# Performance work log

Measured on AMD Instinct MI355X. Metric: run time of the kernel, lower is better.

The kernel has to match this reference:

```python
import jax, jax.numpy as jnp
import numpy as np

N_NODES = 50000
N_EDGES = 800000
IN_FEAT = 100
OUT_FEAT = 100
NUM_RELS = 200
NUM_HEADS = 3
NUM_BASES = 100
SUB_IN = 1   # in_feat // num_bases
SUB_OUT = 1  # out_feat // num_bases


def setup_inputs() -> dict:
    key = jax.random.key(0)
    ks = jax.random.split(key, 10)
    return {
        "h": jax.random.normal(ks[0], (N_NODES, IN_FEAT), jnp.float32),
        "e": jax.random.normal(ks[1], (N_EDGES, IN_FEAT), jnp.float32),
        "norm": jax.random.uniform(ks[2], (N_NODES, 1), jnp.float32),
        "weight": jax.random.normal(ks[3], (NUM_RELS, NUM_BASES * SUB_IN * SUB_OUT), jnp.float32) * 0.1,
        "attn": jax.random.normal(ks[4], (NUM_RELS, NUM_HEADS, OUT_FEAT), jnp.float32) * 0.1,
        "fc_w": jax.random.normal(ks[5], (IN_FEAT, OUT_FEAT * NUM_HEADS), jnp.float32) * 0.1,
        "loop_w": jax.random.normal(ks[6], (IN_FEAT, OUT_FEAT), jnp.float32) * 0.1,
        "rel": jax.random.randint(ks[7], (N_EDGES,), 0, NUM_RELS, jnp.int32),
        "src": jax.random.randint(ks[8], (N_EDGES,), 0, N_NODES, jnp.int32),
        "dst": jax.random.randint(ks[9], (N_EDGES,), 0, N_NODES, jnp.int32),
    }


def reference(h, e, norm, weight, attn, fc_w, loop_w, rel, src, dst):
    E = rel.shape[0]
    # --- relation-indexed block-diagonal message (torch.bmm over blocks) ---
    W_e = weight[rel].reshape(E, NUM_BASES, SUB_IN, SUB_OUT)        # per-edge block weights
    h_src = h[src].reshape(E, NUM_BASES, SUB_IN)                    # gathered src features
    msg = jnp.einsum('ebi,ebio->ebo', h_src, W_e).reshape(E, OUT_FEAT)
    # --- edge-feature attention fuse ---
    a_e = attn[rel]                                                 # (E, H, OUT)
    fc_e = (e @ fc_w).reshape(E, NUM_HEADS, OUT_FEAT)               # fc(edge)
    feat = jax.nn.leaky_relu(a_e * fc_e, 0.2).sum(axis=1)           # (E, OUT)
    msg = msg + feat
    # --- scatter-sum aggregation to dst nodes, then norm + self-loop ---
    agg = jax.ops.segment_sum(msg, dst, num_segments=N_NODES)       # (N, OUT)
    node = agg * norm
    loop_message = h @ loop_w
    return node + loop_message
```

## Files before the change

### kernel.cpp

```cpp
#include <hip/hip_runtime.h>
#include <hip/hip_bf16.h>

#define N_NODES 50000
#define N_EDGES 800000
#define IN_FEAT 100
#define OUT_FEAT 100
#define NUM_RELS 200
#define NUM_HEADS 3

#define KP 128
#define NPH 112
#define MB  128
#define NT_O 7
#define WPB 8
#define MSGW 100
#define BROWS 312
#define HSTRIDE 25600

#define WS_B       0u
#define WS_LW      86016u
#define WS_CNT     114688u
#define WS_OFFS    315392u
#define WS_CURSOR  516096u
#define WS_BSUM    716800u
#define WS_SLOT    717056u
#define WS_META    3917056u
#define WS_MSG     7117056u
#define WS_NEEDED  167117056u
#define NNODES_PAD 50176

typedef __attribute__((ext_vector_type(8))) short short8;
typedef __attribute__((ext_vector_type(4))) float f32x4;

__device__ __forceinline__ unsigned short f2bf(float f) {
    unsigned u = __builtin_bit_cast(unsigned, f);
    unsigned r = u + 0x7FFFu + ((u >> 16) & 1u);
    return (unsigned short)(r >> 16);
}
__device__ __forceinline__ float bf2f(unsigned hs) {
    return __builtin_bit_cast(float, hs << 16);
}

__global__ __launch_bounds__(256) void build_B(const float* __restrict__ fc_w,
                                               unsigned short* __restrict__ Bws) {
    int idx = blockIdx.x * 256 + threadIdx.x;
    if (idx >= BROWS * 16) return;
    int n = idx >> 4, g = idx & 15;
    int head = n / 100, nl = n - head * 100;
    int kt = g >> 2, g4 = g & 3;
    unsigned p[4] = {0u, 0u, 0u, 0u};
    if (n < 300) {
#pragma unroll
        for (int half = 0; half < 2; ++half) {
#pragma unroll
            for (int jp = 0; jp < 2; ++jp) {
                int k_lo = kt * 32 + half * 16 + g4 * 4 + jp * 2;
                int k_hi = k_lo + 1;
                float vlo = (k_lo < IN_FEAT)
                          ? fc_w[k_lo * (OUT_FEAT * NUM_HEADS) + head * OUT_FEAT + nl] : 0.f;
                float vhi = (k_hi < IN_FEAT)
                          ? fc_w[k_hi * (OUT_FEAT * NUM_HEADS) + head * OUT_FEAT + nl] : 0.f;
                p[half * 2 + jp] = (unsigned)f2bf(vlo) | ((unsigned)f2bf(vhi) << 16);
            }
        }
    }
    unsigned off = (unsigned)(n * 256) + (((unsigned)(g * 16)) ^ (((unsigned)(nl & 7)) << 4));
    *reinterpret_cast<int4*>(reinterpret_cast<char*>(Bws) + off) =
        make_int4((int)p[0], (int)p[1], (int)p[2], (int)p[3]);
}

__global__ __launch_bounds__(256) void build_LW(const float* __restrict__ loop_w,
                                                unsigned short* __restrict__ LWws) {
    int idx = blockIdx.x * 256 + threadIdx.x;
    if (idx >= NPH * 16) return;
    int nl = idx >> 4, g = idx & 15;
    int kt = g >> 2, g4 = g & 3;
    unsigned p[4];
#pragma unroll
    for (int half = 0; half < 2; ++half) {
#pragma unroll
        for (int jp = 0; jp < 2; ++jp) {
            int k_lo = kt * 32 + half * 16 + g4 * 4 + jp * 2;
            int k_hi = k_lo + 1;
            float vlo = (k_lo < IN_FEAT && nl < OUT_FEAT) ? loop_w[k_lo * OUT_FEAT + nl] : 0.f;
            float vhi = (k_hi < IN_FEAT && nl < OUT_FEAT) ? loop_w[k_hi * OUT_FEAT + nl] : 0.f;
            p[half * 2 + jp] = (unsigned)f2bf(vlo) | ((unsigned)f2bf(vhi) << 16);
        }
    }
    reinterpret_cast<int4*>(LWws)[idx] = make_int4((int)p[0], (int)p[1], (int)p[2], (int)p[3]);
}

__global__ __launch_bounds__(512, 2) void loop_gemm(const float* __restrict__ h,
                                                    const unsigned short* __restrict__ LWimg,
                                                    float* __restrict__ out) {
    const int tid = threadIdx.x;
    const int wave = tid >> 6, lane = tid & 63;
    const int lrow = lane & 15, lk = lane >> 4;
    const int rbase = blockIdx.x * MB;
    const int grow = rbase + wave * 16 + lrow;
    const bool ok = grow < N_NODES;
    const float* ap = h + (size_t)grow * IN_FEAT;

    short8 afrag[4];
#pragma unroll
    for (int kt = 0; kt < 4; ++kt) {
        int k0 = kt * 32 + lk * 4, k1 = k0 + 16;
        float4 va = (ok && k0 + 4 <= IN_FEAT) ? *reinterpret_cast<const float4*>(ap + k0)
                                              : make_float4(0.f, 0.f, 0.f, 0.f);
        float4 vb = (ok && k1 + 4 <= IN_FEAT) ? *reinterpret_cast<const float4*>(ap + k1)
                                              : make_float4(0.f, 0.f, 0.f, 0.f);
        afrag[kt][0] = (short)f2bf(va.x); afrag[kt][1] = (short)f2bf(va.y);
        afrag[kt][2] = (short)f2bf(va.z); afrag[kt][3] = (short)f2bf(va.w);
        afrag[kt][4] = (short)f2bf(vb.x); afrag[kt][5] = (short)f2bf(vb.y);
        afrag[kt][6] = (short)f2bf(vb.z); afrag[kt][7] = (short)f2bf(vb.w);
    }

#pragma unroll
    for (int nt = 0; nt < NT_O; ++nt) {
        f32x4 acc = (f32x4){0.f, 0.f, 0.f, 0.f};
#pragma unroll
        for (int kt = 0; kt < 4; ++kt) {
            short8 bfrag = *reinterpret_cast<const short8*>(
                LWimg + ((nt * 16 + lrow) * KP + kt * 32 + lk * 8));
            acc = __builtin_amdgcn_mfma_f32_16x16x32_bf16(afrag[kt], bfrag, acc, 0, 0, 0);
        }
        int o = nt * 16 + lrow;
        if (o < OUT_FEAT) {
#pragma unroll
            for (int r = 0; r < 4; ++r) {
                int crow = rbase + wave * 16 + lk * 4 + r;
                if (crow < N_NODES) out[(size_t)crow * OUT_FEAT + o] = acc[r];
            }
        }
    }
}

__global__ __launch_bounds__(512) void hist_kernel(const int* __restrict__ dst,
                                                   int* __restrict__ cnt) {
    int e = blockIdx.x * 512 + threadIdx.x;
    if (e < N_EDGES) atomicAdd(&cnt[dst[e]], 1);
}

__global__ __launch_bounds__(1024) void scan1(const int* __restrict__ cnt,
                                              int* __restrict__ offs,
                                              int* __restrict__ bsum) {
    __shared__ int s[1024];
    int i = blockIdx.x * 1024 + threadIdx.x;
    int v = (i < N_NODES) ? cnt[i] : 0;
    s[threadIdx.x] = v;
    __syncthreads();
    for (int d = 1; d < 1024; d <<= 1) {
        int t = (threadIdx.x >= d) ? s[threadIdx.x - d] : 0;
        __syncthreads();
        s[threadIdx.x] += t;
        __syncthreads();
    }
    offs[i] = s[threadIdx.x] - v;
    if (threadIdx.x == 1023) bsum[blockIdx.x] = s[1023];
}

__global__ __launch_bounds__(64) void scan2(int* __restrict__ bsum) {
    __shared__ int s[64];
    int v = (threadIdx.x < NNODES_PAD / 1024) ? bsum[threadIdx.x] : 0;
    s[threadIdx.x] = v;
    __syncthreads();
    for (int d = 1; d < 64; d <<= 1) {
        int t = (threadIdx.x >= d) ? s[threadIdx.x - d] : 0;
        __syncthreads();
        s[threadIdx.x] += t;
        __syncthreads();
    }
    bsum[threadIdx.x] = s[threadIdx.x] - v;
}

__global__ __launch_bounds__(1024) void scan3(int* __restrict__ offs,
                                              const int* __restrict__ bsum,
                                              int* __restrict__ cursor) {
    int i = blockIdx.x * 1024 + threadIdx.x;
    int v = offs[i] + bsum[blockIdx.x];
    offs[i] = v;
    cursor[i] = v;
}

__global__ __launch_bounds__(512) void scatter_kernel(const int* __restrict__ dst,
                                                      const int* __restrict__ src,
                                                      const int* __restrict__ rel,
                                                      int* __restrict__ cursor,
                                                      int* __restrict__ slotmap,
                                                      int* __restrict__ meta) {
    int e = blockIdx.x * 512 + threadIdx.x;
    if (e < N_EDGES) {
        int p = atomicAdd(&cursor[dst[e]], 1);
        slotmap[e] = p;
        meta[p] = (src[e] & 0xFFFF) | (rel[e] << 16);
    }
}

template<bool TOWS>
__global__ __launch_bounds__(512, 2) void feat_kernel(
        const float* __restrict__ efeat, const int* __restrict__ rel,
        const unsigned short* __restrict__ Bimg, const float* __restrict__ attn,
        const float* __restrict__ h, const float* __restrict__ weight,
        const float* __restrict__ norm, const int* __restrict__ src,
        const int* __restrict__ dst, const int* __restrict__ slotmap,
        float* __restrict__ out, unsigned short* __restrict__ msgws,
        int ntiles) {

    __shared__ __align__(16) unsigned short Blds[BROWS * 128];

    const int tid = threadIdx.x;
    {
        const int4* sp = reinterpret_cast<const int4*>(Bimg);
        int4* dp = reinterpret_cast<int4*>(Blds);
        for (int i = tid; i < BROWS * 128 / 8; i += 512) dp[i] = sp[i];
    }
    __syncthreads();

    const int wave = tid >> 6, lane = tid & 63;
    const int lrow = lane & 15, lk = lane >> 4;
    const int gstride = gridDim.x * WPB;
    int tile = blockIdx.x * WPB + wave;
    if (tile >= ntiles) return;

    const char* Bc = reinterpret_cast<const char*>(Blds);
    int bkt[4];
#pragma unroll
    for (int kt = 0; kt < 4; ++kt)
        bkt[kt] = lrow * 256 + ((kt * 64 + lk * 16) ^ ((lrow & 7) << 4));

    float4 pa[8];
    int prl[4];
    {
        const float* ap = efeat + (size_t)(tile * 16 + lrow) * IN_FEAT;
#pragma unroll
        for (int kt = 0; kt < 4; ++kt) {
            int k0 = kt * 32 + lk * 4, k1 = k0 + 16;
            pa[kt * 2]     = (k0 + 4 <= IN_FEAT) ? *reinterpret_cast<const float4*>(ap + k0)
                                                 : make_float4(0.f, 0.f, 0.f, 0.f);
            pa[kt * 2 + 1] = (k1 + 4 <= IN_FEAT) ? *reinterpret_cast<const float4*>(ap + k1)
                                                 : make_float4(0.f, 0.f, 0.f, 0.f);
        }
        const int* rp = rel + tile * 16 + lk * 4;
#pragma unroll
        for (int r = 0; r < 4; ++r) prl[r] = rp[r];
    }

    while (true) {
        const int cur = tile;
        const int tb = cur * 16;
        short8 afrag[4];
#pragma unroll
        for (int kt = 0; kt < 4; ++kt) {
            float4 va = pa[kt * 2], vb = pa[kt * 2 + 1];
            afrag[kt][0] = (short)f2bf(va.x); afrag[kt][1] = (short)f2bf(va.y);
            afrag[kt][2] = (short)f2bf(va.z); afrag[kt][3] = (short)f2bf(va.w);
            afrag[kt][4] = (short)f2bf(vb.x); afrag[kt][5] = (short)f2bf(vb.y);
            afrag[kt][6] = (short)f2bf(vb.z); afrag[kt][7] = (short)f2bf(vb.w);
        }
        int aoff[4];
#pragma unroll
        for (int r = 0; r < 4; ++r) aoff[r] = prl[r] * (NUM_HEADS * OUT_FEAT);

        int slot_r[4];
        if (TOWS) {
#pragma unroll
            for (int r = 0; r < 4; ++r) slot_r[r] = slotmap[tb + lk * 4 + r];
        }

        int next = tile + gstride;
        bool more = next < ntiles;
        {
            int pidx = more ? next : cur;
            const float* ap = efeat + (size_t)(pidx * 16 + lrow) * IN_FEAT;
#pragma unroll
            for (int kt = 0; kt < 4; ++kt) {
                int k0 = kt * 32 + lk * 4, k1 = k0 + 16;
                pa[kt * 2]     = (k0 + 4 <= IN_FEAT) ? *reinterpret_cast<const float4*>(ap + k0)
                                                     : make_float4(0.f, 0.f, 0.f, 0.f);
                pa[kt * 2 + 1] = (k1 + 4 <= IN_FEAT) ? *reinterpret_cast<const float4*>(ap + k1)
                                                     : make_float4(0.f, 0.f, 0.f, 0.f);
            }
            const int* rp = rel + pidx * 16 + lk * 4;
#pragma unroll
            for (int r = 0; r < 4; ++r) prl[r] = rp[r];
        }

        float feat[NT_O][4];
#pragma unroll
        for (int nt = 0; nt < NT_O; ++nt)
#pragma unroll
            for (int r = 0; r < 4; ++r) feat[nt][r] = 0.f;

#pragma unroll 1
        for (int hh = 0; hh < NUM_HEADS; ++hh) {
            const char* Bh = Bc + hh * HSTRIDE;
#pragma unroll
            for (int nt = 0; nt < NT_O; ++nt) {
                f32x4 acc = (f32x4){0.f, 0.f, 0.f, 0.f};
#pragma unroll
                for (int kt = 0; kt < 4; ++kt) {
                    short8 bfrag = *reinterpret_cast<const short8*>(
                        Bh + bkt[kt] + nt * 4096);
                    acc = __builtin_amdgcn_mfma_f32_16x16x32_bf16(afrag[kt], bfrag, acc, 0, 0, 0);
                }
                int o = nt * 16 + lrow;
                if (o < OUT_FEAT) {
                    int oo = hh * OUT_FEAT + o;
#pragma unroll
                    for (int r = 0; r < 4; ++r) {
                        float v = acc[r] * attn[aoff[r] + oo];
                        feat[nt][r] += (v > 0.f) ? v : 0.2f * v;
                    }
                }
            }
        }

        if (TOWS) {
#pragma unroll
            for (int nt = 0; nt < NT_O; ++nt) {
                int o = nt * 16 + lrow;
                if (o < OUT_FEAT) {
#pragma unroll
                    for (int r = 0; r < 4; ++r)
                        msgws[(size_t)slot_r[r] * MSGW + o] = f2bf(feat[nt][r]);
                }
            }
        } else {
            int sr_r[4], d_r[4]; float nm_r[4]; int rl_r[4];
#pragma unroll
            for (int r = 0; r < 4; ++r) {
                int ei = tb + lk * 4 + r;
                sr_r[r] = src[ei]; d_r[r] = dst[ei]; nm_r[r] = norm[d_r[r]];
                rl_r[r] = aoff[r] / (NUM_HEADS * OUT_FEAT);
            }
#pragma unroll
            for (int nt = 0; nt < NT_O; ++nt) {
                int o = nt * 16 + lrow;
                if (o < OUT_FEAT) {
#pragma unroll
                    for (int r = 0; r < 4; ++r) {
                        float mg = h[(size_t)sr_r[r] * IN_FEAT + o] *
                                   weight[(size_t)rl_r[r] * OUT_FEAT + o];
                        atomicAdd(&out[(size_t)d_r[r] * OUT_FEAT + o],
                                  (mg + feat[nt][r]) * nm_r[r]);
                    }
                }
            }
        }

        if (!more) break;
        tile = next;
    }
}

__global__ __launch_bounds__(256, 4) void agg_kernel(
        const unsigned short* __restrict__ msgws, const int* __restrict__ offs,
        const int* __restrict__ cnt, const int* __restrict__ meta,
        const float* __restrict__ h, const float* __restrict__ weight,
        const float* __restrict__ norm, float* __restrict__ out) {
    int wv = threadIdx.x >> 6, lane = threadIdx.x & 63;
    int n = blockIdx.x * 4 + wv;
    if (n >= N_NODES) return;
    int start = offs[n], deg = cnt[n];
    if (deg == 0 || lane >= OUT_FEAT / 2) return;
    const unsigned* mp = reinterpret_cast<const unsigned*>(msgws);
    float ax = 0.f, ay = 0.f;
    int k = start, end = start + deg;
    for (; k + 2 <= end; k += 2) {
        int m0 = meta[k], m1 = meta[k + 1];
        int s0 = m0 & 0xFFFF, s1 = m1 & 0xFFFF;
        int r0 = (unsigned)m0 >> 16, r1 = (unsigned)m1 >> 16;
        unsigned u0 = mp[(size_t)k * (MSGW / 2) + lane];
        unsigned u1 = mp[(size_t)(k + 1) * (MSGW / 2) + lane];
        float2 h0 = *reinterpret_cast<const float2*>(h + (size_t)s0 * IN_FEAT + 2 * lane);
        float2 w0 = *reinterpret_cast<const float2*>(weight + (size_t)r0 * OUT_FEAT + 2 * lane);
        float2 h1 = *reinterpret_cast<const float2*>(h + (size_t)s1 * IN_FEAT + 2 * lane);
        float2 w1 = *reinterpret_cast<const float2*>(weight + (size_t)r1 * OUT_FEAT + 2 * lane);
        ax += h0.x * w0.x + bf2f(u0 & 0xffffu) + h1.x * w1.x + bf2f(u1 & 0xffffu);
        ay += h0.y * w0.y + bf2f(u0 >> 16) + h1.y * w1.y + bf2f(u1 >> 16);
    }
    if (k < end) {
        int m0 = meta[k];
        int s0 = m0 & 0xFFFF, r0 = (unsigned)m0 >> 16;
        unsigned u0 = mp[(size_t)k * (MSGW / 2) + lane];
        float2 h0 = *reinterpret_cast<const float2*>(h + (size_t)s0 * IN_FEAT + 2 * lane);
        float2 w0 = *reinterpret_cast<const float2*>(weight + (size_t)r0 * OUT_FEAT + 2 * lane);
        ax += h0.x * w0.x + bf2f(u0 & 0xffffu);
        ay += h0.y * w0.y + bf2f(u0 >> 16);
    }
    float nm = norm[n];
    float2* op = reinterpret_cast<float2*>(out + (size_t)n * OUT_FEAT) + lane;
    float2 curv = *op;
    curv.x += ax * nm; curv.y += ay * nm;
    *op = curv;
}

extern "C" void kernel_launch(void* const* d_in, const int* in_sizes, int n_in,
                              void* d_out, int out_size, void* d_ws, size_t ws_size,
                              hipStream_t stream) {
    const float* h      = (const float*)d_in[0];
    const float* efeat  = (const float*)d_in[1];
    const float* norm   = (const float*)d_in[2];
    const float* weight = (const float*)d_in[3];
    const float* attn   = (const float*)d_in[4];
    const float* fc_w   = (const float*)d_in[5];
    const float* loop_w = (const float*)d_in[6];
    const int*   rel    = (const int*)d_in[7];
    const int*   src    = (const int*)d_in[8];
    const int*   dst    = (const int*)d_in[9];
    float* out = (float*)d_out;

    char* ws = (char*)d_ws;
    unsigned short* Bimg  = (unsigned short*)(ws + WS_B);
    unsigned short* LWimg = (unsigned short*)(ws + WS_LW);
    int* cnt     = (int*)(ws + WS_CNT);
    int* offs    = (int*)(ws + WS_OFFS);
    int* cursor  = (int*)(ws + WS_CURSOR);
    int* bsum    = (int*)(ws + WS_BSUM);
    int* slotmap = (int*)(ws + WS_SLOT);
    int* meta    = (int*)(ws + WS_META);
    unsigned short* msgws = (unsigned short*)(ws + WS_MSG);

    build_B<<<(BROWS * 16 + 255) / 256, 256, 0, stream>>>(fc_w, Bimg);
    build_LW<<<(NPH * 16 + 255) / 256, 256, 0, stream>>>(loop_w, LWimg);
    loop_gemm<<<(N_NODES + MB - 1) / MB, 512, 0, stream>>>(h, LWimg, out);

    const int ntiles = N_EDGES / 16;

    if (ws_size >= (size_t)WS_NEEDED) {
        hipMemsetAsync(cnt, 0, NNODES_PAD * sizeof(int), stream);
        hist_kernel<<<(N_EDGES + 511) / 512, 512, 0, stream>>>(dst, cnt);
        scan1<<<NNODES_PAD / 1024, 1024, 0, stream>>>(cnt, offs, bsum);
        scan2<<<1, 64, 0, stream>>>(bsum);
        scan3<<<NNODES_PAD / 1024, 1024, 0, stream>>>(offs, bsum, cursor);
        scatter_kernel<<<(N_EDGES + 511) / 512, 512, 0, stream>>>(
            dst, src, rel, cursor, slotmap, meta);

        feat_kernel<true><<<512, 512, 0, stream>>>(
            efeat, rel, Bimg, attn, h, weight, norm, src, dst, slotmap,
            out, msgws, ntiles);
        agg_kernel<<<(N_NODES + 3) / 4, 256, 0, stream>>>(
            msgws, offs, cnt, meta, h, weight, norm, out);
    } else {
        feat_kernel<false><<<512, 512, 0, stream>>>(
            efeat, rel, Bimg, attn, h, weight, norm, src, dst, nullptr,
            out, msgws, ntiles);
    }
}
```

Measured before the change: 407.4 us.

## Move h*weight message and norm into feat kernel; drop meta array

The relation-weighted h[src] term and the destination norm are now computed in the edge feature kernel and folded into the bf16 message before it is written. The aggregation kernel then only sums messages, with 4-way unrolling, and the scatter kernel no longer builds the packed src/rel meta array. The feature kernel also switches to 1024-thread blocks with 16 waves and one block per CU. This cuts random gathers and meta traffic in the aggregation phase but adds scalar h/weight/norm gathers to the edge kernel and rounds the full message, including the h*weight term, to bf16.

```diff
diff --git a/kernel.cpp b/kernel.cpp
--- a/kernel.cpp
+++ b/kernel.cpp
@@ -12,7 +12,7 @@
 #define NPH 112
 #define MB  128
 #define NT_O 7
-#define WPB 8
+#define WPB 16
 #define MSGW 100
 #define BROWS 312
 #define HSTRIDE 25600
@@ -24,7 +24,6 @@
 #define WS_CURSOR  516096u
 #define WS_BSUM    716800u
 #define WS_SLOT    717056u
-#define WS_META    3917056u
 #define WS_MSG     7117056u
 #define WS_NEEDED  167117056u
 #define NNODES_PAD 50176
@@ -183,21 +182,17 @@
 }
 
 __global__ __launch_bounds__(512) void scatter_kernel(const int* __restrict__ dst,
-                                                      const int* __restrict__ src,
-                                                      const int* __restrict__ rel,
                                                       int* __restrict__ cursor,
-                                                      int* __restrict__ slotmap,
-                                                      int* __restrict__ meta) {
+                                                      int* __restrict__ slotmap) {
     int e = blockIdx.x * 512 + threadIdx.x;
     if (e < N_EDGES) {
         int p = atomicAdd(&cursor[dst[e]], 1);
         slotmap[e] = p;
-        meta[p] = (src[e] & 0xFFFF) | (rel[e] << 16);
     }
 }
 
 template<bool TOWS>
-__global__ __launch_bounds__(512, 2) void feat_kernel(
+__global__ __launch_bounds__(1024, 1) void feat_kernel(
         const float* __restrict__ efeat, const int* __restrict__ rel,
         const unsigned short* __restrict__ Bimg, const float* __restrict__ attn,
         const float* __restrict__ h, const float* __restrict__ weight,
@@ -212,7 +207,7 @@
     {
         const int4* sp = reinterpret_cast<const int4*>(Bimg);
         int4* dp = reinterpret_cast<int4*>(Blds);
-        for (int i = tid; i < BROWS * 128 / 8; i += 512) dp[i] = sp[i];
+        for (int i = tid; i < BROWS * 128 / 8; i += 1024) dp[i] = sp[i];
     }
     __syncthreads();
 
@@ -229,9 +224,11 @@
         bkt[kt] = lrow * 256 + ((kt * 64 + lk * 16) ^ ((lrow & 7) << 4));
 
     float4 pa[8];
-    int prl[4];
-    {
-        const float* ap = efeat + (size_t)(tile * 16 + lrow) * IN_FEAT;
+    int prl[4], psr[4], pdd[4];
+
+    auto prefetch = [&](int t) {
+        int eb = t * 16;
+        const float* ap = efeat + (size_t)(eb + lrow) * IN_FEAT;
 #pragma unroll
         for (int kt = 0; kt < 4; ++kt) {
             int k0 = kt * 32 + lk * 4, k1 = k0 + 16;
@@ -240,14 +237,19 @@
             pa[kt * 2 + 1] = (k1 + 4 <= IN_FEAT) ? *reinterpret_cast<const float4*>(ap + k1)
                                                  : make_float4(0.f, 0.f, 0.f, 0.f);
         }
-        const int* rp = rel + tile * 16 + lk * 4;
-#pragma unroll
-        for (int r = 0; r < 4; ++r) prl[r] = rp[r];
-    }
+        const int* rp = rel + eb + lk * 4;
+        const int* sp = src + eb + lk * 4;
+        const int* dp = dst + eb + lk * 4;
+#pragma unroll
+        for (int r = 0; r < 4; ++r) { prl[r] = rp[r]; psr[r] = sp[r]; pdd[r] = dp[r]; }
+    };
+
+    prefetch(tile);
 
     while (true) {
         const int cur = tile;
         const int tb = cur * 16;
+
         short8 afrag[4];
 #pragma unroll
         for (int kt = 0; kt < 4; ++kt) {
@@ -257,39 +259,36 @@
             afrag[kt][4] = (short)f2bf(vb.x); afrag[kt][5] = (short)f2bf(vb.y);
             afrag[kt][6] = (short)f2bf(vb.z); afrag[kt][7] = (short)f2bf(vb.w);
         }
-        int aoff[4];
-#pragma unroll
-        for (int r = 0; r < 4; ++r) aoff[r] = prl[r] * (NUM_HEADS * OUT_FEAT);
-
-        int slot_r[4];
+        int aoff[4], hoff[4], woff[4];
+        float nm[4];
+#pragma unroll
+        for (int r = 0; r < 4; ++r) {
+            aoff[r] = prl[r] * (NUM_HEADS * OUT_FEAT);
+            woff[r] = prl[r] * OUT_FEAT;
+            hoff[r] = psr[r] * IN_FEAT;
+            nm[r]   = norm[pdd[r]];
+        }
+        int slot_r[4], dd_r[4];
         if (TOWS) {
 #pragma unroll
             for (int r = 0; r < 4; ++r) slot_r[r] = slotmap[tb + lk * 4 + r];
+        } else {
+#pragma unroll
+            for (int r = 0; r < 4; ++r) dd_r[r] = pdd[r];
         }
 
         int next = tile + gstride;
         bool more = next < ntiles;
-        {
-            int pidx = more ? next : cur;
-            const float* ap = efeat + (size_t)(pidx * 16 + lrow) * IN_FEAT;
-#pragma unroll
-            for (int kt = 0; kt < 4; ++kt) {
-                int k0 = kt * 32 + lk * 4, k1 = k0 + 16;
-                pa[kt * 2]     = (k0 + 4 <= IN_FEAT) ? *reinterpret_cast<const float4*>(ap + k0)
-                                                     : make_float4(0.f, 0.f, 0.f, 0.f);
-                pa[kt * 2 + 1] = (k1 + 4 <= IN_FEAT) ? *reinterpret_cast<const float4*>(ap + k1)
-                                                     : make_float4(0.f, 0.f, 0.f, 0.f);
-            }
-            const int* rp = rel + pidx * 16 + lk * 4;
-#pragma unroll
-            for (int r = 0; r < 4; ++r) prl[r] = rp[r];
-        }
+        prefetch(more ? next : cur);
 
         float feat[NT_O][4];
 #pragma unroll
-        for (int nt = 0; nt < NT_O; ++nt)
-#pragma unroll
-            for (int r = 0; r < 4; ++r) feat[nt][r] = 0.f;
+        for (int nt = 0; nt < NT_O; ++nt) {
+            int o = nt * 16 + lrow;
+#pragma unroll
+            for (int r = 0; r < 4; ++r)
+                feat[nt][r] = (o < OUT_FEAT) ? h[hoff[r] + o] * weight[woff[r] + o] : 0.f;
+        }
 
 #pragma unroll 1
         for (int hh = 0; hh < NUM_HEADS; ++hh) {
@@ -322,28 +321,18 @@
                 if (o < OUT_FEAT) {
 #pragma unroll
                     for (int r = 0; r < 4; ++r)
-                        msgws[(size_t)slot_r[r] * MSGW + o] = f2bf(feat[nt][r]);
+                        msgws[(size_t)slot_r[r] * MSGW + o] = f2bf(feat[nt][r] * nm[r]);
                 }
             }
         } else {
-            int sr_r[4], d_r[4]; float nm_r[4]; int rl_r[4];
-#pragma unroll
-            for (int r = 0; r < 4; ++r) {
-                int ei = tb + lk * 4 + r;
-                sr_r[r] = src[ei]; d_r[r] = dst[ei]; nm_r[r] = norm[d_r[r]];
-                rl_r[r] = aoff[r] / (NUM_HEADS * OUT_FEAT);
-            }
 #pragma unroll
             for (int nt = 0; nt < NT_O; ++nt) {
                 int o = nt * 16 + lrow;
                 if (o < OUT_FEAT) {
 #pragma unroll
-                    for (int r = 0; r < 4; ++r) {
-                        float mg = h[(size_t)sr_r[r] * IN_FEAT + o] *
-                                   weight[(size_t)rl_r[r] * OUT_FEAT + o];
-                        atomicAdd(&out[(size_t)d_r[r] * OUT_FEAT + o],
-                                  (mg + feat[nt][r]) * nm_r[r]);
-                    }
+                    for (int r = 0; r < 4; ++r)
+                        atomicAdd(&out[(size_t)dd_r[r] * OUT_FEAT + o],
+                                  feat[nt][r] * nm[r]);
                 }
             }
         }
@@ -355,9 +344,7 @@
 
 __global__ __launch_bounds__(256, 4) void agg_kernel(
         const unsigned short* __restrict__ msgws, const int* __restrict__ offs,
-        const int* __restrict__ cnt, const int* __restrict__ meta,
-        const float* __restrict__ h, const float* __restrict__ weight,
-        const float* __restrict__ norm, float* __restrict__ out) {
+        const int* __restrict__ cnt, float* __restrict__ out) {
     int wv = threadIdx.x >> 6, lane = threadIdx.x & 63;
     int n = blockIdx.x * 4 + wv;
     if (n >= N_NODES) return;
@@ -366,32 +353,22 @@
     const unsigned* mp = reinterpret_cast<const unsigned*>(msgws);
     float ax = 0.f, ay = 0.f;
     int k = start, end = start + deg;
-    for (; k + 2 <= end; k += 2) {
-        int m0 = meta[k], m1 = meta[k + 1];
-        int s0 = m0 & 0xFFFF, s1 = m1 & 0xFFFF;
-        int r0 = (unsigned)m0 >> 16, r1 = (unsigned)m1 >> 16;
+    for (; k + 4 <= end; k += 4) {
         unsigned u0 = mp[(size_t)k * (MSGW / 2) + lane];
         unsigned u1 = mp[(size_t)(k + 1) * (MSGW / 2) + lane];
-        float2 h0 = *reinterpret_cast<const float2*>(h + (size_t)s0 * IN_FEAT + 2 * lane);
-        float2 w0 = *reinterpret_cast<const float2*>(weight + (size_t)r0 * OUT_FEAT + 2 * lane);
-        float2 h1 = *reinterpret_cast<const float2*>(h + (size_t)s1 * IN_FEAT + 2 * lane);
-        float2 w1 = *reinterpret_cast<const float2*>(weight + (size_t)r1 * OUT_FEAT + 2 * lane);
-        ax += h0.x * w0.x + bf2f(u0 & 0xffffu) + h1.x * w1.x + bf2f(u1 & 0xffffu);
-        ay += h0.y * w0.y + bf2f(u0 >> 16) + h1.y * w1.y + bf2f(u1 >> 16);
-    }
-    if (k < end) {
-        int m0 = meta[k];
-        int s0 = m0 & 0xFFFF, r0 = (unsigned)m0 >> 16;
+        unsigned u2 = mp[(size_t)(k + 2) * (MSGW / 2) + lane];
+        unsigned u3 = mp[(size_t)(k + 3) * (MSGW / 2) + lane];
+        ax += bf2f(u0 & 0xffffu) + bf2f(u1 & 0xffffu) + bf2f(u2 & 0xffffu) + bf2f(u3 & 0xffffu);
+        ay += bf2f(u0 >> 16) + bf2f(u1 >> 16) + bf2f(u2 >> 16) + bf2f(u3 >> 16);
+    }
+    for (; k < end; ++k) {
         unsigned u0 = mp[(size_t)k * (MSGW / 2) + lane];
-        float2 h0 = *reinterpret_cast<const float2*>(h + (size_t)s0 * IN_FEAT + 2 * lane);
-        float2 w0 = *reinterpret_cast<const float2*>(weight + (size_t)r0 * OUT_FEAT + 2 * lane);
-        ax += h0.x * w0.x + bf2f(u0 & 0xffffu);
-        ay += h0.y * w0.y + bf2f(u0 >> 16);
-    }
-    float nm = norm[n];
+        ax += bf2f(u0 & 0xffffu);
+        ay += bf2f(u0 >> 16);
+    }
     float2* op = reinterpret_cast<float2*>(out + (size_t)n * OUT_FEAT) + lane;
     float2 curv = *op;
-    curv.x += ax * nm; curv.y += ay * nm;
+    curv.x += ax; curv.y += ay;
     *op = curv;
 }
 
@@ -418,7 +395,6 @@
     int* cursor  = (int*)(ws + WS_CURSOR);
     int* bsum    = (int*)(ws + WS_BSUM);
     int* slotmap = (int*)(ws + WS_SLOT);
-    int* meta    = (int*)(ws + WS_META);
     unsigned short* msgws = (unsigned short*)(ws + WS_MSG);
 
     build_B<<<(BROWS * 16 + 255) / 256, 256, 0, stream>>>(fc_w, Bimg);
@@ -433,16 +409,14 @@
         scan1<<<NNODES_PAD / 1024, 1024, 0, stream>>>(cnt, offs, bsum);
         scan2<<<1, 64, 0, stream>>>(bsum);
         scan3<<<NNODES_PAD / 1024, 1024, 0, stream>>>(offs, bsum, cursor);
-        scatter_kernel<<<(N_EDGES + 511) / 512, 512, 0, stream>>>(
-            dst, src, rel, cursor, slotmap, meta);
-
-        feat_kernel<true><<<512, 512, 0, stream>>>(
+        scatter_kernel<<<(N_EDGES + 511) / 512, 512, 0, stream>>>(dst, cursor, slotmap);
+
+        feat_kernel<true><<<256, 1024, 0, stream>>>(
             efeat, rel, Bimg, attn, h, weight, norm, src, dst, slotmap,
             out, msgws, ntiles);
-        agg_kernel<<<(N_NODES + 3) / 4, 256, 0, stream>>>(
-            msgws, offs, cnt, meta, h, weight, norm, out);
+        agg_kernel<<<(N_NODES + 3) / 4, 256, 0, stream>>>(msgws, offs, cnt, out);
     } else {
-        feat_kernel<false><<<512, 512, 0, stream>>>(
+        feat_kernel<false><<<256, 1024, 0, stream>>>(
             efeat, rel, Bimg, attn, h, weight, norm, src, dst, nullptr,
             out, msgws, ntiles);
     }
```

Result: slower. 702.4 us (+72.4%).
